# Kernel optimization log

Hardware: AMD Instinct MI355X
Metric: run time of the kernel (lower is better)

## Reference

```python
import jax, jax.numpy as jnp
import numpy as np

B = 32768   # batch
M = 8       # movements
P = 4       # phases
H = 64      # MOVEMENT_HIDDEN
E = 64      # MOVEMENT_EMB
R = 32      # RELATION_DIM
PH = 128    # PAIR_HIDDEN
PHASE_MOVEMENTS = [[0, 1], [2, 3], [4, 5], [6, 7]]


def _linear_params(k, fin, fout):
    lim = 1.0 / np.sqrt(fin)
    kw, kb = jax.random.split(k)
    W = jax.random.uniform(kw, (fin, fout), jnp.float32, -lim, lim)
    b = jax.random.uniform(kb, (fout,), jnp.float32, -lim, lim)
    return W, b


def setup_inputs() -> dict:
    key = jax.random.key(0)
    ks = jax.random.split(key, 12)
    movement_counts = jax.random.uniform(ks[0], (B, M), jnp.float32) * 30.0
    phase = jax.random.randint(ks[1], (B,), 0, P)
    cur_phase_onehot = jax.nn.one_hot(phase, P, dtype=jnp.float32)
    Wv, bv = _linear_params(ks[2], 1, H)
    Ws, bs = _linear_params(ks[3], 1, H)
    Wm, bm = _linear_params(ks[4], 2 * H, E)
    relation_table = jax.random.normal(ks[5], (P, P, R), jnp.float32) * 0.1
    Wd1, bd1 = _linear_params(ks[6], 2 * E, PH)
    Wd2, bd2 = _linear_params(ks[7], PH, PH)
    Wr1, br1 = _linear_params(ks[8], R, PH)
    Wr2, br2 = _linear_params(ks[9], PH, PH)
    Wc, bc = _linear_params(ks[10], PH, 1)
    return {
        "movement_counts": movement_counts, "cur_phase_onehot": cur_phase_onehot,
        "Wv": Wv, "bv": bv, "Ws": Ws, "bs": bs, "Wm": Wm, "bm": bm,
        "relation_table": relation_table,
        "Wd1": Wd1, "bd1": bd1, "Wd2": Wd2, "bd2": bd2,
        "Wr1": Wr1, "br1": br1, "Wr2": Wr2, "br2": br2,
        "Wc": Wc, "bc": bc,
    }


def _movement_to_phase():
    m2p = np.zeros((M, P), np.float32)
    for p_idx, moves in enumerate(PHASE_MOVEMENTS):
        for mv in moves:
            m2p[mv, p_idx] = 1.0
    return jnp.asarray(m2p)


def reference(movement_counts, cur_phase_onehot, Wv, bv, Ws, bs, Wm, bm,
              relation_table, Wd1, bd1, Wd2, bd2, Wr1, br1, Wr2, br2, Wc, bc):
    Bb = movement_counts.shape[0]
    m2p = _movement_to_phase()                       # (M, P)
    # phase one-hot -> per-movement bit
    s_mov = cur_phase_onehot @ m2p.T                 # (B, M)
    # per-movement scalar -> hidden (Linear on scalar input == outer product)
    h_v = jax.nn.relu(movement_counts[..., None] * Wv[0] + bv)   # (B, M, H)
    h_s = jax.nn.relu(s_mov[..., None] * Ws[0] + bs)             # (B, M, H)
    d_i = jax.nn.relu(jnp.concatenate([h_v, h_s], -1) @ Wm + bm)  # (B, M, E)
    # sum movement embeddings per phase; lay out phase-major to mirror torch's cat-along-batch
    d_p = jnp.einsum('bme,mp->pbe', d_i, m2p)        # (P, B, E)
    # all P x P ordered phase pairs, concatenated demand vectors
    Dpq = jnp.concatenate([
        jnp.broadcast_to(d_p[:, None], (P, P, Bb, E)),
        jnp.broadcast_to(d_p[None, :], (P, P, Bb, E)),
    ], axis=-1)                                      # (P, P, B, 2E)
    Hd = jax.nn.relu(Dpq @ Wd1 + bd1)
    Hd = jax.nn.relu(Hd @ Wd2 + bd2)                 # (P, P, B, PH)
    # relation embedding per pair (batch-broadcast, same math as expand)
    Er = relation_table[:, :, None, :]               # (P, P, 1, R)
    Hr = jax.nn.relu(Er @ Wr1 + br1)
    Hr = jax.nn.relu(Hr @ Wr2 + br2)                 # (P, P, 1, PH)
    Hc = Hd * Hr                                     # (P, P, B, PH)
    Cpqb = jax.nn.relu(Hc @ Wc + bc)[..., 0]         # (P, P, B)
    # torch builds C_flat in (pair-major, batch-minor) order then reshapes to (B,P,P)
    C = Cpqb.reshape(-1).reshape(Bb, P, P)
    return jnp.sum(C, axis=2)                        # (B, P)
```

## Files before the change

kernel.cpp:

```cpp
#include <hip/hip_runtime.h>

#define NT   512
#define NBLK 4096

typedef _Float16 half8 __attribute__((ext_vector_type(8)));
typedef _Float16 half4 __attribute__((ext_vector_type(4)));
typedef unsigned short us8 __attribute__((ext_vector_type(8)));
typedef float    f32x4 __attribute__((ext_vector_type(4)));

#define L_AH   0
#define L_DPH  2048
#define L_UV   3072
#define S_BD1  7168
#define S_BD2  7296
#define S_C0   7424
#define S_C1   7488
#define S_SP   7552
#define LDS_FLOATS 7808

#define WS_CS   2048
#define WS_W2F  2304
#define WS_W1F  10496
#define WS_WMF  18688

__global__ void frap_setup(const float* __restrict__ Ws0, const float* __restrict__ bs,
                           const float* __restrict__ Wm,  const float* __restrict__ bm,
                           const float* __restrict__ rel, const float* __restrict__ Wr1,
                           const float* __restrict__ br1, const float* __restrict__ Wr2,
                           const float* __restrict__ br2, const float* __restrict__ Wc,
                           const float* __restrict__ Wd1, const float* __restrict__ Wd2,
                           float* __restrict__ wsf)
{
    __shared__ float hr1[128];
    const int t = threadIdx.x;
    if (blockIdx.x == 16) {
        const int s = t >> 6, e = t & 63;
        float acc = bm[e];
        for (int h = 0; h < 64; ++h) {
            float hs = fmaxf((s ? Ws0[h] : 0.0f) + bs[h], 0.0f);
            acc = fmaf(hs, Wm[(64 + h) * 64 + e], acc);
        }
        wsf[WS_CS + s * 64 + e] = acc;
    } else if (blockIdx.x == 17) {
        for (int idx = t; idx < 2048; idx += 128) {
            const int l = idx & 63, f = idx >> 6;
            const int jt32 = f >> 3, nt = f & 7;
            half8 v;
#pragma unroll
            for (int kk = 0; kk < 8; ++kk)
                v[kk] = (_Float16)Wd2[(jt32 * 32 + (l >> 4) * 8 + kk) * 128 + nt * 16 + (l & 15)];
            *(half8*)((char*)wsf + WS_W2F * 4 + idx * 16) = v;
        }
    } else if (blockIdx.x == 18) {
        for (int idx = t; idx < 2048; idx += 128) {
            const int l = idx & 63, f = idx >> 6;
            const int half = f >> 4, ks = (f >> 3) & 1, jt = f & 7;
            half8 v;
#pragma unroll
            for (int kk = 0; kk < 8; ++kk)
                v[kk] = (_Float16)Wd1[(half * 64 + ks * 32 + (l >> 4) * 8 + kk) * 128 + jt * 16 + (l & 15)];
            *(half8*)((char*)wsf + WS_W1F * 4 + idx * 16) = v;
        }
    } else if (blockIdx.x == 19) {
        for (int f = t; f < 512; f += 128) {
            const int l = f & 63, ks = (f >> 6) & 1, tile = f >> 7;
            const int kbase = (ks * 4 + (l >> 4)) * 8, col = tile * 16 + (l & 15);
            half8 v;
#pragma unroll
            for (int kk = 0; kk < 8; ++kk)
                v[kk] = (_Float16)Wm[(kbase + kk) * 64 + col];
            *(half8*)((char*)wsf + WS_WMF * 4 + f * 16) = v;
        }
    } else {
        const int pair = blockIdx.x;
        float a = br1[t];
        for (int r = 0; r < 32; ++r) a = fmaf(rel[pair * 32 + r], Wr1[r * 128 + t], a);
        hr1[t] = fmaxf(a, 0.0f);
        __syncthreads();
        float a2 = br2[t];
        for (int j = 0; j < 128; ++j) a2 = fmaf(hr1[j], Wr2[j * 128 + t], a2);
        wsf[pair * 128 + t] = fmaxf(a2, 0.0f) * Wc[t];
    }
}

__global__ __launch_bounds__(NT, 6)
void frap_main(const float* __restrict__ mc_g, const float* __restrict__ oh_g,
               const float* __restrict__ Wv_g, const float* __restrict__ bv_g,
               const float* __restrict__ bd1_g, const float* __restrict__ bd2_g,
               const float* __restrict__ bc_g,
               const float* __restrict__ wsf, float* __restrict__ out)
{
    extern __shared__ float lds[];
    const int t = threadIdx.x;
    const int wv = t >> 6, ln = t & 63;
    const int bid = blockIdx.x;

    if (t < 128) lds[S_BD1 + t] = bd1_g[t];
    else if (t < 256) lds[S_BD2 + (t - 128)] = bd2_g[t - 128];
    else if (t < 384) lds[S_C0 + (t - 256)] = wsf[WS_CS + (t - 256)];
    const float bcv = bc_g[0];

    {
        const int r = t >> 3, h8 = (t & 7) * 8;
        const float mcv = mc_g[bid * 64 + r];
        float4 wa = *(const float4*)&Wv_g[h8];
        float4 wb = *(const float4*)&Wv_g[h8 + 4];
        float4 ba = *(const float4*)&bv_g[h8];
        float4 bb = *(const float4*)&bv_g[h8 + 4];
        half8 v;
        v[0] = (_Float16)fmaxf(fmaf(mcv, wa.x, ba.x), 0.f);
        v[1] = (_Float16)fmaxf(fmaf(mcv, wa.y, ba.y), 0.f);
        v[2] = (_Float16)fmaxf(fmaf(mcv, wa.z, ba.z), 0.f);
        v[3] = (_Float16)fmaxf(fmaf(mcv, wa.w, ba.w), 0.f);
        v[4] = (_Float16)fmaxf(fmaf(mcv, wb.x, bb.x), 0.f);
        v[5] = (_Float16)fmaxf(fmaf(mcv, wb.y, bb.y), 0.f);
        v[6] = (_Float16)fmaxf(fmaf(mcv, wb.z, bb.z), 0.f);
        v[7] = (_Float16)fmaxf(fmaf(mcv, wb.w, bb.w), 0.f);
        *(half8*)((char*)lds + L_AH * 4 + r * 128 + (((t & 7) ^ (r & 7)) << 4)) = v;
    }
    __syncthreads();

    const int lr = ln & 15, lq = ln >> 4;

    {
        const int rt1 = wv & 3, ch = wv >> 2;
        f32x4 acc[2];
        acc[0] = (f32x4){0.f, 0.f, 0.f, 0.f};
        acc[1] = (f32x4){0.f, 0.f, 0.f, 0.f};
#pragma unroll
        for (int ks = 0; ks < 2; ++ks) {
            const int c8 = ks * 4 + lq;
            const int r = rt1 * 16 + lr;
            half8 af = *(half8*)((char*)lds + L_AH * 4 + r * 128 + ((c8 ^ (r & 7)) << 4));
#pragma unroll
            for (int cti = 0; cti < 2; ++cti) {
                const int tile = ch * 2 + cti;
                half8 bf = *(const half8*)((const char*)wsf + WS_WMF * 4
                                           + ((tile * 2 + ks) * 64 + ln) * 16);
                acc[cti] = __builtin_amdgcn_mfma_f32_16x16x32_f16(af, bf, acc[cti], 0, 0, 0);
            }
        }
        const int bloc = rt1 * 2 + (lq >> 1);
#pragma unroll
        for (int pp = 0; pp < 2; ++pp) {
            const int p = (lq & 1) * 2 + pp;
            const float sv = oh_g[(bid * 8 + bloc) * 4 + p];
            const int csb = (sv > 0.5f) ? S_C1 : S_C0;
            const int row32 = p * 8 + bloc, sw = row32 & 7;
#pragma unroll
            for (int cti = 0; cti < 2; ++cti) {
                const int e = (ch * 2 + cti) * 16 + lr;
                const float cs = lds[csb + e];
                float d0 = fmaxf(acc[cti][2 * pp] + cs, 0.f);
                float d1 = fmaxf(acc[cti][2 * pp + 1] + cs, 0.f);
                *(_Float16*)((char*)lds + L_DPH * 4 + row32 * 128
                             + (((e >> 3) ^ sw) << 4) + (e & 7) * 2) = (_Float16)(d0 + d1);
            }
        }
    }
    __syncthreads();

    {
        const int half = wv & 1, ct = (wv >> 1) & 1, jh = wv >> 2;
        const int row32 = ct * 16 + lr;
        f32x4 uvacc[4];
#pragma unroll
        for (int j4 = 0; j4 < 4; ++j4) {
            if (half == 0)
                uvacc[j4] = *(f32x4*)&lds[S_BD1 + (jh * 4 + j4) * 16 + lq * 4];
            else
                uvacc[j4] = (f32x4){0.f, 0.f, 0.f, 0.f};
        }
#pragma unroll
        for (int ks = 0; ks < 2; ++ks) {
            half8 bfr = *(half8*)((char*)lds + L_DPH * 4 + row32 * 128
                                  + (((ks * 4 + lq) ^ (lr & 7)) << 4));
#pragma unroll
            for (int j4 = 0; j4 < 4; ++j4) {
                half8 afr = *(const half8*)((const char*)wsf + WS_W1F * 4
                            + (((half * 2 + ks) * 8 + jh * 4 + j4) * 64 + ln) * 16);
                uvacc[j4] = __builtin_amdgcn_mfma_f32_16x16x32_f16(afr, bfr, uvacc[j4], 0, 0, 0);
            }
        }
        const int csw = row32 & 7;
        char* base = (char*)lds + L_UV * 4 + half * 8192 + row32 * 256 + (lq & 1) * 8;
#pragma unroll
        for (int j4 = 0; j4 < 4; ++j4) {
            const int jt = jh * 4 + j4;
            f32x4 v = uvacc[j4];
            half4 hv;
            hv[0] = (_Float16)v[0]; hv[1] = (_Float16)v[1];
            hv[2] = (_Float16)v[2]; hv[3] = (_Float16)v[3];
            *(half4*)(base + (((jt * 2 + (lq >> 1)) ^ csw) << 4)) = hv;
        }
    }
    __syncthreads();

    const int rth = wv & 3, nh = wv >> 2;
    const int rt0 = rth * 2;
    const int ucol = rth * 8 + (lr & 7);
    const int vcol0 = lr;
    const int vcol1 = 16 + lr;
    char* ub  = (char*)lds + L_UV * 4 + ucol * 256;
    char* vb0 = (char*)lds + L_UV * 4 + 8192 + vcol0 * 256;
    char* vb1 = (char*)lds + L_UV * 4 + 8192 + vcol1 * 256;

    f32x4 acc2[2][4];
#pragma unroll
    for (int ntl = 0; ntl < 4; ++ntl) {
        f32x4 b2 = *(f32x4*)&lds[S_BD2 + (nh * 4 + ntl) * 16 + lq * 4];
        acc2[0][ntl] = b2;
        acc2[1][ntl] = b2;
    }

#pragma unroll
    for (int jt32 = 0; jt32 < 4; ++jt32) {
        const int ch = jt32 * 4 + lq;
        half8 w2[4];
#pragma unroll
        for (int ntl = 0; ntl < 4; ++ntl)
            w2[ntl] = *(const half8*)((const char*)wsf + WS_W2F * 4
                                      + ((jt32 * 8 + nh * 4 + ntl) * 64 + ln) * 16);
        half8 u  = *(half8*)(ub  + ((ch ^ (ucol & 7)) << 4));
        half8 v0 = *(half8*)(vb0 + ((ch ^ (vcol0 & 7)) << 4));
        half8 v1 = *(half8*)(vb1 + ((ch ^ (vcol1 & 7)) << 4));
        half8 s0 = u + v0;
        half8 s1 = u + v1;
#if __has_builtin(__builtin_elementwise_max)
        half8 z = {};
        s0 = __builtin_elementwise_max(s0, z);
        s1 = __builtin_elementwise_max(s1, z);
#else
        us8 b0 = __builtin_bit_cast(us8, s0);
        us8 m0 = (b0 >> 15) - (us8)1; b0 &= m0;
        s0 = __builtin_bit_cast(half8, b0);
        us8 b1 = __builtin_bit_cast(us8, s1);
        us8 m1 = (b1 >> 15) - (us8)1; b1 &= m1;
        s1 = __builtin_bit_cast(half8, b1);
#endif
#pragma unroll
        for (int ntl = 0; ntl < 4; ++ntl) {
            acc2[0][ntl] = __builtin_amdgcn_mfma_f32_16x16x32_f16(w2[ntl], s0, acc2[0][ntl], 0, 0, 0);
            acc2[1][ntl] = __builtin_amdgcn_mfma_f32_16x16x32_f16(w2[ntl], s1, acc2[1][ntl], 0, 0, 0);
        }
    }

#pragma unroll
    for (int i = 0; i < 2; ++i) {
        const int pair = (rt0 + i) * 2 + (lr >> 3);
        const float* wcr = &wsf[pair * 128 + lq * 4];
        float tot = 0.f;
#pragma unroll
        for (int ntl = 0; ntl < 4; ++ntl) {
            f32x4 wc = *(const f32x4*)&wcr[(nh * 4 + ntl) * 16];
#pragma unroll
            for (int r2 = 0; r2 < 4; ++r2)
                tot = fmaf(fmaxf(acc2[i][ntl][r2], 0.f), wc[r2], tot);
        }
        tot += __shfl_xor(tot, 16, 64);
        tot += __shfl_xor(tot, 32, 64);
        if (lq == 0)
            lds[S_SP + nh * 128 + (rt0 + i) * 16 + lr] = tot;
    }
    __syncthreads();

    if (t < 32) {
        const int r0 = t * 4;
        float o = 0.f;
#pragma unroll
        for (int d = 0; d < 4; ++d) {
            const int r = r0 + d;
            o += fmaxf(lds[S_SP + r] + lds[S_SP + 128 + r] + bcv, 0.f);
        }
        out[(r0 >> 5) * 32768 + ((r0 >> 3) & 3) * 8192 + bid * 2 + ((r0 & 7) >> 2)] = o;
    }
}

extern "C" void kernel_launch(void* const* d_in, const int* in_sizes, int n_in,
                              void* d_out, int out_size, void* d_ws, size_t ws_size,
                              hipStream_t stream) {
    (void)in_sizes; (void)n_in; (void)out_size; (void)ws_size;
    const float* mc  = (const float*)d_in[0];
    const float* oh  = (const float*)d_in[1];
    const float* Wv  = (const float*)d_in[2];
    const float* bv  = (const float*)d_in[3];
    const float* Ws  = (const float*)d_in[4];
    const float* bs  = (const float*)d_in[5];
    const float* Wm  = (const float*)d_in[6];
    const float* bm  = (const float*)d_in[7];
    const float* rel = (const float*)d_in[8];
    const float* Wd1 = (const float*)d_in[9];
    const float* bd1 = (const float*)d_in[10];
    const float* Wd2 = (const float*)d_in[11];
    const float* bd2 = (const float*)d_in[12];
    const float* Wr1 = (const float*)d_in[13];
    const float* br1 = (const float*)d_in[14];
    const float* Wr2 = (const float*)d_in[15];
    const float* br2 = (const float*)d_in[16];
    const float* Wc  = (const float*)d_in[17];
    const float* bc  = (const float*)d_in[18];
    float* wsf = (float*)d_ws;
    float* out = (float*)d_out;

    hipLaunchKernelGGL(frap_setup, dim3(20), dim3(128), 0, stream,
                       Ws, bs, Wm, bm, rel, Wr1, br1, Wr2, br2, Wc, Wd1, Wd2, wsf);
    hipLaunchKernelGGL(frap_main, dim3(NBLK), dim3(NT), LDS_FLOATS * 4, stream,
                       mc, oh, Wv, bv, bd1, bd2, bc, wsf, out);
}
```

Baseline: 53.66 us.

## Process two batch tiles per block to reuse weight fragments across tiles

Each block now handles two 8-row batch sub-tiles instead of one, halving the grid to 2048 blocks. The Wm, Wd1 and Wd2 MFMA weight fragments loaded from global memory are reused for both sub-tiles, and the LDS layout is doubled to hold both tiles' intermediates. This cuts per-block fixed overhead and weight reloads. In exchange it roughly doubles LDS and accumulator registers per block and lowers the occupancy hint from 6 to 2 blocks per CU, which can reduce latency hiding.

```diff
diff --git a/kernel.cpp b/kernel.cpp
--- a/kernel.cpp
+++ b/kernel.cpp
@@ -1,7 +1,7 @@
 #include <hip/hip_runtime.h>
 
 #define NT   512
-#define NBLK 4096
+#define NBLK 2048
 
 typedef _Float16 half8 __attribute__((ext_vector_type(8)));
 typedef _Float16 half4 __attribute__((ext_vector_type(4)));
@@ -9,14 +9,14 @@
 typedef float    f32x4 __attribute__((ext_vector_type(4)));
 
 #define L_AH   0
-#define L_DPH  2048
-#define L_UV   3072
-#define S_BD1  7168
-#define S_BD2  7296
-#define S_C0   7424
-#define S_C1   7488
-#define S_SP   7552
-#define LDS_FLOATS 7808
+#define L_DPH  4096
+#define L_UV   6144
+#define S_BD1  14336
+#define S_BD2  14464
+#define S_C0   14592
+#define S_C1   14656
+#define S_SP   14720
+#define LDS_FLOATS 15232
 
 #define WS_CS   2048
 #define WS_W2F  2304
@@ -83,7 +83,7 @@
     }
 }
 
-__global__ __launch_bounds__(NT, 6)
+__global__ __launch_bounds__(NT, 2)
 void frap_main(const float* __restrict__ mc_g, const float* __restrict__ oh_g,
                const float* __restrict__ Wv_g, const float* __restrict__ bv_g,
                const float* __restrict__ bd1_g, const float* __restrict__ bd2_g,
@@ -102,21 +102,25 @@
 
     {
         const int r = t >> 3, h8 = (t & 7) * 8;
-        const float mcv = mc_g[bid * 64 + r];
         float4 wa = *(const float4*)&Wv_g[h8];
         float4 wb = *(const float4*)&Wv_g[h8 + 4];
         float4 ba = *(const float4*)&bv_g[h8];
         float4 bb = *(const float4*)&bv_g[h8 + 4];
-        half8 v;
-        v[0] = (_Float16)fmaxf(fmaf(mcv, wa.x, ba.x), 0.f);
-        v[1] = (_Float16)fmaxf(fmaf(mcv, wa.y, ba.y), 0.f);
-        v[2] = (_Float16)fmaxf(fmaf(mcv, wa.z, ba.z), 0.f);
-        v[3] = (_Float16)fmaxf(fmaf(mcv, wa.w, ba.w), 0.f);
-        v[4] = (_Float16)fmaxf(fmaf(mcv, wb.x, bb.x), 0.f);
-        v[5] = (_Float16)fmaxf(fmaf(mcv, wb.y, bb.y), 0.f);
-        v[6] = (_Float16)fmaxf(fmaf(mcv, wb.z, bb.z), 0.f);
-        v[7] = (_Float16)fmaxf(fmaf(mcv, wb.w, bb.w), 0.f);
-        *(half8*)((char*)lds + L_AH * 4 + r * 128 + (((t & 7) ^ (r & 7)) << 4)) = v;
+#pragma unroll
+        for (int s = 0; s < 2; ++s) {
+            const float mcv = mc_g[bid * 128 + s * 64 + r];
+            half8 v;
+            v[0] = (_Float16)fmaxf(fmaf(mcv, wa.x, ba.x), 0.f);
+            v[1] = (_Float16)fmaxf(fmaf(mcv, wa.y, ba.y), 0.f);
+            v[2] = (_Float16)fmaxf(fmaf(mcv, wa.z, ba.z), 0.f);
+            v[3] = (_Float16)fmaxf(fmaf(mcv, wa.w, ba.w), 0.f);
+            v[4] = (_Float16)fmaxf(fmaf(mcv, wb.x, bb.x), 0.f);
+            v[5] = (_Float16)fmaxf(fmaf(mcv, wb.y, bb.y), 0.f);
+            v[6] = (_Float16)fmaxf(fmaf(mcv, wb.z, bb.z), 0.f);
+            v[7] = (_Float16)fmaxf(fmaf(mcv, wb.w, bb.w), 0.f);
+            *(half8*)((char*)lds + L_AH * 4 + s * 8192 + r * 128
+                      + (((t & 7) ^ (r & 7)) << 4)) = v;
+        }
     }
     __syncthreads();
 
@@ -124,37 +128,50 @@
 
     {
         const int rt1 = wv & 3, ch = wv >> 2;
-        f32x4 acc[2];
-        acc[0] = (f32x4){0.f, 0.f, 0.f, 0.f};
-        acc[1] = (f32x4){0.f, 0.f, 0.f, 0.f};
-#pragma unroll
-        for (int ks = 0; ks < 2; ++ks) {
-            const int c8 = ks * 4 + lq;
-            const int r = rt1 * 16 + lr;
-            half8 af = *(half8*)((char*)lds + L_AH * 4 + r * 128 + ((c8 ^ (r & 7)) << 4));
-#pragma unroll
-            for (int cti = 0; cti < 2; ++cti) {
-                const int tile = ch * 2 + cti;
-                half8 bf = *(const half8*)((const char*)wsf + WS_WMF * 4
-                                           + ((tile * 2 + ks) * 64 + ln) * 16);
-                acc[cti] = __builtin_amdgcn_mfma_f32_16x16x32_f16(af, bf, acc[cti], 0, 0, 0);
+        half8 bf[2][2];
+#pragma unroll
+        for (int ks = 0; ks < 2; ++ks)
+#pragma unroll
+            for (int cti = 0; cti < 2; ++cti)
+                bf[ks][cti] = *(const half8*)((const char*)wsf + WS_WMF * 4
+                              + (((ch * 2 + cti) * 2 + ks) * 64 + ln) * 16);
+        f32x4 acc[2][2];
+#pragma unroll
+        for (int s = 0; s < 2; ++s)
+#pragma unroll
+            for (int cti = 0; cti < 2; ++cti)
+                acc[s][cti] = (f32x4){0.f, 0.f, 0.f, 0.f};
+#pragma unroll
+        for (int s = 0; s < 2; ++s) {
+#pragma unroll
+            for (int ks = 0; ks < 2; ++ks) {
+                const int c8 = ks * 4 + lq;
+                const int r = rt1 * 16 + lr;
+                half8 af = *(half8*)((char*)lds + L_AH * 4 + s * 8192 + r * 128
+                                     + ((c8 ^ (r & 7)) << 4));
+#pragma unroll
+                for (int cti = 0; cti < 2; ++cti)
+                    acc[s][cti] = __builtin_amdgcn_mfma_f32_16x16x32_f16(af, bf[ks][cti], acc[s][cti], 0, 0, 0);
             }
         }
         const int bloc = rt1 * 2 + (lq >> 1);
 #pragma unroll
-        for (int pp = 0; pp < 2; ++pp) {
-            const int p = (lq & 1) * 2 + pp;
-            const float sv = oh_g[(bid * 8 + bloc) * 4 + p];
-            const int csb = (sv > 0.5f) ? S_C1 : S_C0;
-            const int row32 = p * 8 + bloc, sw = row32 & 7;
-#pragma unroll
-            for (int cti = 0; cti < 2; ++cti) {
-                const int e = (ch * 2 + cti) * 16 + lr;
-                const float cs = lds[csb + e];
-                float d0 = fmaxf(acc[cti][2 * pp] + cs, 0.f);
-                float d1 = fmaxf(acc[cti][2 * pp + 1] + cs, 0.f);
-                *(_Float16*)((char*)lds + L_DPH * 4 + row32 * 128
-                             + (((e >> 3) ^ sw) << 4) + (e & 7) * 2) = (_Float16)(d0 + d1);
+        for (int s = 0; s < 2; ++s) {
+#pragma unroll
+            for (int pp = 0; pp < 2; ++pp) {
+                const int p = (lq & 1) * 2 + pp;
+                const float sv = oh_g[(bid * 16 + s * 8 + bloc) * 4 + p];
+                const int csb = (sv > 0.5f) ? S_C1 : S_C0;
+                const int row32 = p * 8 + bloc, sw = row32 & 7;
+#pragma unroll
+                for (int cti = 0; cti < 2; ++cti) {
+                    const int e = (ch * 2 + cti) * 16 + lr;
+                    const float cs = lds[csb + e];
+                    float d0 = fmaxf(acc[s][cti][2 * pp] + cs, 0.f);
+                    float d1 = fmaxf(acc[s][cti][2 * pp + 1] + cs, 0.f);
+                    *(_Float16*)((char*)lds + L_DPH * 4 + s * 4096 + row32 * 128
+                                 + (((e >> 3) ^ sw) << 4) + (e & 7) * 2) = (_Float16)(d0 + d1);
+                }
             }
         }
     }
@@ -163,35 +180,46 @@
     {
         const int half = wv & 1, ct = (wv >> 1) & 1, jh = wv >> 2;
         const int row32 = ct * 16 + lr;
-        f32x4 uvacc[4];
-#pragma unroll
-        for (int j4 = 0; j4 < 4; ++j4) {
-            if (half == 0)
-                uvacc[j4] = *(f32x4*)&lds[S_BD1 + (jh * 4 + j4) * 16 + lq * 4];
-            else
-                uvacc[j4] = (f32x4){0.f, 0.f, 0.f, 0.f};
-        }
+        f32x4 uvacc[2][4];
+#pragma unroll
+        for (int s = 0; s < 2; ++s)
+#pragma unroll
+            for (int j4 = 0; j4 < 4; ++j4) {
+                if (half == 0)
+                    uvacc[s][j4] = *(f32x4*)&lds[S_BD1 + (jh * 4 + j4) * 16 + lq * 4];
+                else
+                    uvacc[s][j4] = (f32x4){0.f, 0.f, 0.f, 0.f};
+            }
 #pragma unroll
         for (int ks = 0; ks < 2; ++ks) {
-            half8 bfr = *(half8*)((char*)lds + L_DPH * 4 + row32 * 128
-                                  + (((ks * 4 + lq) ^ (lr & 7)) << 4));
+            half8 bfr[2];
+#pragma unroll
+            for (int s = 0; s < 2; ++s)
+                bfr[s] = *(half8*)((char*)lds + L_DPH * 4 + s * 4096 + row32 * 128
+                                   + (((ks * 4 + lq) ^ (lr & 7)) << 4));
 #pragma unroll
             for (int j4 = 0; j4 < 4; ++j4) {
                 half8 afr = *(const half8*)((const char*)wsf + WS_W1F * 4
                             + (((half * 2 + ks) * 8 + jh * 4 + j4) * 64 + ln) * 16);
-                uvacc[j4] = __builtin_amdgcn_mfma_f32_16x16x32_f16(afr, bfr, uvacc[j4], 0, 0, 0);
+#pragma unroll
+                for (int s = 0; s < 2; ++s)
+                    uvacc[s][j4] = __builtin_amdgcn_mfma_f32_16x16x32_f16(afr, bfr[s], uvacc[s][j4], 0, 0, 0);
             }
         }
         const int csw = row32 & 7;
-        char* base = (char*)lds + L_UV * 4 + half * 8192 + row32 * 256 + (lq & 1) * 8;
-#pragma unroll
-        for (int j4 = 0; j4 < 4; ++j4) {
-            const int jt = jh * 4 + j4;
-            f32x4 v = uvacc[j4];
-            half4 hv;
-            hv[0] = (_Float16)v[0]; hv[1] = (_Float16)v[1];
-            hv[2] = (_Float16)v[2]; hv[3] = (_Float16)v[3];
-            *(half4*)(base + (((jt * 2 + (lq >> 1)) ^ csw) << 4)) = hv;
+#pragma unroll
+        for (int s = 0; s < 2; ++s) {
+            char* base = (char*)lds + L_UV * 4 + s * 16384 + half * 8192
+                         + row32 * 256 + (lq & 1) * 8;
+#pragma unroll
+            for (int j4 = 0; j4 < 4; ++j4) {
+                const int jt = jh * 4 + j4;
+                f32x4 v = uvacc[s][j4];
+                half4 hv;
+                hv[0] = (_Float16)v[0]; hv[1] = (_Float16)v[1];
+                hv[2] = (_Float16)v[2]; hv[3] = (_Float16)v[3];
+                *(half4*)(base + (((jt * 2 + (lq >> 1)) ^ csw) << 4)) = hv;
+            }
         }
     }
     __syncthreads();
@@ -201,16 +229,13 @@
     const int ucol = rth * 8 + (lr & 7);
     const int vcol0 = lr;
     const int vcol1 = 16 + lr;
-    char* ub  = (char*)lds + L_UV * 4 + ucol * 256;
-    char* vb0 = (char*)lds + L_UV * 4 + 8192 + vcol0 * 256;
-    char* vb1 = (char*)lds + L_UV * 4 + 8192 + vcol1 * 256;
-
-    f32x4 acc2[2][4];
+
+    f32x4 acc2[2][2][4];
 #pragma unroll
     for (int ntl = 0; ntl < 4; ++ntl) {
         f32x4 b2 = *(f32x4*)&lds[S_BD2 + (nh * 4 + ntl) * 16 + lq * 4];
-        acc2[0][ntl] = b2;
-        acc2[1][ntl] = b2;
+        acc2[0][0][ntl] = b2; acc2[0][1][ntl] = b2;
+        acc2[1][0][ntl] = b2; acc2[1][1][ntl] = b2;
     }
 
 #pragma unroll
@@ -221,27 +246,31 @@
         for (int ntl = 0; ntl < 4; ++ntl)
             w2[ntl] = *(const half8*)((const char*)wsf + WS_W2F * 4
                                       + ((jt32 * 8 + nh * 4 + ntl) * 64 + ln) * 16);
-        half8 u  = *(half8*)(ub  + ((ch ^ (ucol & 7)) << 4));
-        half8 v0 = *(half8*)(vb0 + ((ch ^ (vcol0 & 7)) << 4));
-        half8 v1 = *(half8*)(vb1 + ((ch ^ (vcol1 & 7)) << 4));
-        half8 s0 = u + v0;
-        half8 s1 = u + v1;
+#pragma unroll
+        for (int s = 0; s < 2; ++s) {
+            char* uvb = (char*)lds + L_UV * 4 + s * 16384;
+            half8 u  = *(half8*)(uvb + ucol * 256 + ((ch ^ (ucol & 7)) << 4));
+            half8 v0 = *(half8*)(uvb + 8192 + vcol0 * 256 + ((ch ^ (vcol0 & 7)) << 4));
+            half8 v1 = *(half8*)(uvb + 8192 + vcol1 * 256 + ((ch ^ (vcol1 & 7)) << 4));
+            half8 s0 = u + v0;
+            half8 s1 = u + v1;
 #if __has_builtin(__builtin_elementwise_max)
-        half8 z = {};
-        s0 = __builtin_elementwise_max(s0, z);
-        s1 = __builtin_elementwise_max(s1, z);
+            half8 z = {};
+            s0 = __builtin_elementwise_max(s0, z);
+            s1 = __builtin_elementwise_max(s1, z);
 #else
-        us8 b0 = __builtin_bit_cast(us8, s0);
-        us8 m0 = (b0 >> 15) - (us8)1; b0 &= m0;
-        s0 = __builtin_bit_cast(half8, b0);
-        us8 b1 = __builtin_bit_cast(us8, s1);
-        us8 m1 = (b1 >> 15) - (us8)1; b1 &= m1;
-        s1 = __builtin_bit_cast(half8, b1);
+            us8 b0 = __builtin_bit_cast(us8, s0);
+            us8 m0 = (b0 >> 15) - (us8)1; b0 &= m0;
+            s0 = __builtin_bit_cast(half8, b0);
+            us8 b1 = __builtin_bit_cast(us8, s1);
+            us8 m1 = (b1 >> 15) - (us8)1; b1 &= m1;
+            s1 = __builtin_bit_cast(half8, b1);
 #endif
 #pragma unroll
-        for (int ntl = 0; ntl < 4; ++ntl) {
-            acc2[0][ntl] = __builtin_amdgcn_mfma_f32_16x16x32_f16(w2[ntl], s0, acc2[0][ntl], 0, 0, 0);
-            acc2[1][ntl] = __builtin_amdgcn_mfma_f32_16x16x32_f16(w2[ntl], s1, acc2[1][ntl], 0, 0, 0);
+            for (int ntl = 0; ntl < 4; ++ntl) {
+                acc2[s][0][ntl] = __builtin_amdgcn_mfma_f32_16x16x32_f16(w2[ntl], s0, acc2[s][0][ntl], 0, 0, 0);
+                acc2[s][1][ntl] = __builtin_amdgcn_mfma_f32_16x16x32_f16(w2[ntl], s1, acc2[s][1][ntl], 0, 0, 0);
+            }
         }
     }
 
@@ -249,30 +278,36 @@
     for (int i = 0; i < 2; ++i) {
         const int pair = (rt0 + i) * 2 + (lr >> 3);
         const float* wcr = &wsf[pair * 128 + lq * 4];
-        float tot = 0.f;
-#pragma unroll
-        for (int ntl = 0; ntl < 4; ++ntl) {
-            f32x4 wc = *(const f32x4*)&wcr[(nh * 4 + ntl) * 16];
-#pragma unroll
-            for (int r2 = 0; r2 < 4; ++r2)
-                tot = fmaf(fmaxf(acc2[i][ntl][r2], 0.f), wc[r2], tot);
-        }
-        tot += __shfl_xor(tot, 16, 64);
-        tot += __shfl_xor(tot, 32, 64);
-        if (lq == 0)
-            lds[S_SP + nh * 128 + (rt0 + i) * 16 + lr] = tot;
+        f32x4 wc[4];
+#pragma unroll
+        for (int ntl = 0; ntl < 4; ++ntl)
+            wc[ntl] = *(const f32x4*)&wcr[(nh * 4 + ntl) * 16];
+#pragma unroll
+        for (int s = 0; s < 2; ++s) {
+            float tot = 0.f;
+#pragma unroll
+            for (int ntl = 0; ntl < 4; ++ntl)
+#pragma unroll
+                for (int r2 = 0; r2 < 4; ++r2)
+                    tot = fmaf(fmaxf(acc2[s][i][ntl][r2], 0.f), wc[ntl][r2], tot);
+            tot += __shfl_xor(tot, 16, 64);
+            tot += __shfl_xor(tot, 32, 64);
+            if (lq == 0)
+                lds[S_SP + s * 256 + nh * 128 + (rt0 + i) * 16 + lr] = tot;
+        }
     }
     __syncthreads();
 
-    if (t < 32) {
-        const int r0 = t * 4;
+    if (t < 64) {
+        const int s = t >> 5, tt = t & 31;
+        const int r0 = tt * 4;
         float o = 0.f;
 #pragma unroll
         for (int d = 0; d < 4; ++d) {
             const int r = r0 + d;
-            o += fmaxf(lds[S_SP + r] + lds[S_SP + 128 + r] + bcv, 0.f);
-        }
-        out[(r0 >> 5) * 32768 + ((r0 >> 3) & 3) * 8192 + bid * 2 + ((r0 & 7) >> 2)] = o;
+            o += fmaxf(lds[S_SP + s * 256 + r] + lds[S_SP + s * 256 + 128 + r] + bcv, 0.f);
+        }
+        out[(r0 >> 5) * 32768 + ((r0 >> 3) & 3) * 8192 + (bid * 2 + s) * 2 + ((r0 & 7) >> 2)] = o;
     }
 }
 
```

Result: faster. 43.94 us, median of 2 (-18.1%).
